# Kernel optimization log

Hardware: AMD Instinct MI355X
Metric: run time of the kernel (lower is better)

The kernel has to match this reference:

```python
import jax, jax.numpy as jnp
import numpy as np

MU = 255          # mu-law levels - 1
H = 64            # block_hidden_size
SKIP = 256        # skip_size
NL = 24           # num_layers
CYC = 6           # cycle_size -> dilation = 2**(i % CYC)
UPK = 4           # upsample conv kernel/stride
REP = 75          # upsample repeat
LF = 80           # local_features_size
B = 2
LLEN = 64                      # local (spectrogram) frames
SLEN = LLEN * UPK * REP        # 19200 signal samples


def setup_inputs() -> dict:
    key = jax.random.key(0)
    ks = jax.random.split(key, 16)
    s = 0.1
    rn = lambda k, shape: jax.random.normal(k, shape, jnp.float32) * s
    return {
        "local_features": jax.random.normal(ks[0], (B, LLEN, LF), jnp.float32),
        "gold_signal": jax.random.randint(ks[1], (B, SLEN), 0, MU + 1, jnp.int32),
        "embed_W": rn(ks[2], (H, MU + 1)),          # 1x1 conv (mu+1 -> H), as matrix
        "embed_b": rn(ks[3], (H,)),
        "up_W": rn(ks[4], (LF, LF, UPK)),           # ConvTranspose1d weight [in, out, k]
        "up_b": rn(ks[5], (LF,)),
        "cond_W": rn(ks[6], (NL * 2 * H, LF)),      # 1x1 conv LF -> NL*2H
        "cond_b": rn(ks[7], (NL * 2 * H,)),
        "dil_W": rn(ks[8], (NL, 2 * H, H, 2)),      # dilated causal conv, kernel 2
        "dil_b": rn(ks[9], (NL, 2 * H)),
        "skip_W": rn(ks[10], (NL, SKIP, H)),
        "skip_b": rn(ks[11], (NL, SKIP)),
        "res_W": rn(ks[12], (NL - 1, H, H)),        # no residual conv on last layer
        "res_b": rn(ks[13], (NL - 1, H)),
        "out_W1": rn(ks[14], (MU + 1, SKIP)),       # out conv 1 (no bias)
        "out_W2": rn(ks[15], (MU + 1, MU + 1)),     # out conv 2 (no bias)
    }


def reference(local_features, gold_signal, embed_W, embed_b, up_W, up_b,
              cond_W, cond_b, dil_W, dil_b, skip_W, skip_b, res_W, res_b,
              out_W1, out_W2):
    Bv = local_features.shape[0]
    # --- conditional features upsample ---
    x = jnp.transpose(local_features, (0, 2, 1))                     # [B, LF, Lloc]
    # ConvTranspose1d with kernel == stride == UPK: each frame emits UPK frames
    up = jnp.einsum('bct,cok->botk', x, up_W).reshape(Bv, LF, -1)    # [B, LF, Lloc*UPK]
    up = up + up_b[None, :, None]
    up = jnp.repeat(up, REP, axis=-1)                                # [B, LF, SLEN]
    cond = jnp.einsum('oc,bct->bot', cond_W, up) + cond_b[None, :, None]
    L = cond.shape[-1]
    cond = cond.reshape(Bv, NL, 2 * H, L)                            # per-layer 2H channels
    # --- embed mu-law one-hot signal (one-hot matmul == gather) ---
    sig = jnp.transpose(embed_W[:, gold_signal], (1, 0, 2)) + embed_b[None, :, None]  # [B, H, L]
    # --- residual blocks ---
    skip_sum = jnp.zeros((Bv, SKIP, L), cond.dtype)
    for i in range(NL):
        d = 2 ** (i % CYC)
        prev = jnp.pad(sig, ((0, 0), (0, 0), (d, 0)))[:, :, :L]      # causal shift by dilation
        a = (jnp.einsum('oc,bct->bot', dil_W[i, :, :, 0], prev)
             + jnp.einsum('oc,bct->bot', dil_W[i, :, :, 1], sig)
             + dil_b[i][None, :, None] + cond[:, i])
        z = jnp.tanh(a[:, :H]) * jax.nn.sigmoid(a[:, H:])            # gated activation
        skip_sum = skip_sum + jnp.einsum('oc,bct->bot', skip_W[i], z) + skip_b[i][None, :, None]
        if i < NL - 1:
            sig = sig + jnp.einsum('oc,bct->bot', res_W[i], z) + res_b[i][None, :, None]
    # --- output head: ReLU -> 1x1 -> ReLU -> 1x1 -> log_softmax over levels ---
    h = jax.nn.relu(skip_sum)
    h = jax.nn.relu(jnp.einsum('oc,bct->bot', out_W1, h))
    logits = jnp.einsum('oc,bct->bot', out_W2, h)
    return jax.nn.log_softmax(logits, axis=1)                        # [B, mu+1, SLEN]
```

## Files before the change

### kernel.cpp

```cpp
#include <hip/hip_runtime.h>
#include <math.h>

#define MU1   256
#define H     64
#define H2    128
#define SKIPC 256
#define NL    24
#define LF    80
#define UPK   4
#define REP   75
#define BB    2
#define LLEN  64
#define LL    19200

using bf16x8 = __attribute__((ext_vector_type(8))) short;
using bf16x4 = __attribute__((ext_vector_type(4))) short;
using f32x4  = __attribute__((ext_vector_type(4))) float;

__device__ __forceinline__ float b2f(short s) {
    union { unsigned u; float f; } v; v.u = ((unsigned)(unsigned short)s) << 16; return v.f;
}
__device__ __forceinline__ short f2b(float f) {
    union { float f; unsigned u; } v; v.f = f;
    unsigned r = (v.u + 0x7fff + ((v.u >> 16) & 1)) >> 16;
    return (short)r;
}

__global__ __launch_bounds__(256) void prep_kernel(
    const float* __restrict__ dil_W,  const float* __restrict__ skip_W,
    const float* __restrict__ res_W,  const float* __restrict__ embed_W,
    const float* __restrict__ embed_b,const float* __restrict__ cond_W,
    const float* __restrict__ out_W1, const float* __restrict__ out_W2,
    const float* __restrict__ skip_b,
    short* __restrict__ dil_Wb, short* __restrict__ skip_Wb,
    short* __restrict__ res_Wb, short* __restrict__ embed_allb,
    float* __restrict__ cond_Wt, short* __restrict__ W1b,
    short* __restrict__ W2b, float* __restrict__ sbsum)
{
    int idx = blockIdx.x * 256 + threadIdx.x;
    const int n1 = NL * 2 * H2 * H;
    const int n2 = NL * SKIPC * H;
    const int n3 = (NL - 1) * H * H;
    const int n4 = MU1 * H;
    const int n5 = LF * NL * H2;
    const int n6 = MU1 * SKIPC;
    const int n7 = MU1 * MU1;
    if (idx < n1) {
        int c = idx & 63; int o = (idx >> 6) & 127;
        int k = (idx >> 13) & 1; int i = idx >> 14;
        dil_Wb[idx] = f2b(dil_W[((i * H2 + o) * H + c) * 2 + k]);
        return;
    }
    idx -= n1;
    if (idx < n2) { skip_Wb[idx] = f2b(skip_W[idx]); return; }
    idx -= n2;
    if (idx < n3) { res_Wb[idx] = f2b(res_W[idx]); return; }
    idx -= n3;
    if (idx < n4) {
        int h = idx & 63; int g = idx >> 6;
        embed_allb[idx] = f2b(embed_W[h * MU1 + g] + embed_b[h]);
        return;
    }
    idx -= n4;
    if (idx < n5) {
        int o = idx % (NL * H2); int c = idx / (NL * H2);
        cond_Wt[idx] = cond_W[o * LF + c];
        return;
    }
    idx -= n5;
    if (idx < n6) { W1b[idx] = f2b(out_W1[idx]); return; }
    idx -= n6;
    if (idx < n7) { W2b[idx] = f2b(out_W2[idx]); return; }
    idx -= n7;
    if (idx < SKIPC) {
        float a = 0.f;
        for (int i = 0; i < NL; i++) a += skip_b[i * SKIPC + idx];
        sbsum[idx] = a;
        return;
    }
}

__global__ __launch_bounds__(256) void embed_kernel(
    const int* __restrict__ gold, const short* __restrict__ eW,
    short* __restrict__ sig)
{
    int idx = blockIdx.x * 256 + threadIdx.x;
    if (idx >= BB * LL * 8) return;
    int ch = idx & 7; int bt = idx >> 3;
    int g = gold[bt];
    *(bf16x8*)(sig + (size_t)bt * H + ch * 8) = *(const bf16x8*)(eW + g * H + ch * 8);
}

__global__ __launch_bounds__(256) void cond_kernel(
    const float* __restrict__ lf, const float* __restrict__ up_W,
    const float* __restrict__ up_b, const float* __restrict__ cond_Wt,
    const float* __restrict__ cond_b, const float* __restrict__ dil_b,
    float* __restrict__ condS)
{
    __shared__ float s_up[LF];
    int j = blockIdx.x;
    int ot = blockIdx.y;
    int b = blockIdx.z;
    int frame = j >> 2, k = j & 3;
    int tid = threadIdx.x;
    if (tid < LF) {
        float a = up_b[tid];
        const float* lfr = lf + (b * LLEN + frame) * LF;
        #pragma unroll 8
        for (int c = 0; c < LF; ++c) a += lfr[c] * up_W[(c * LF + tid) * UPK + k];
        s_up[tid] = a;
    }
    __syncthreads();
    int o = ot * 256 + tid;
    float a = cond_b[o] + dil_b[o];
    #pragma unroll 8
    for (int c = 0; c < LF; ++c) a += cond_Wt[c * 3072 + o] * s_up[c];
    condS[((size_t)(b * 256 + j)) * 3072 + o] = a;
}

template<bool LASTPAIR>
__global__ __launch_bounds__(256) void pair_mfma(
    const short* __restrict__ sig_in, short* __restrict__ sig_out,
    short* __restrict__ z_grp,
    const short* __restrict__ dil_Wb_all,
    const short* __restrict__ res_Wb_all,
    const float* __restrict__ res_b_all,
    const float* __restrict__ condS,
    int p, int dA, int dB)
{
    __shared__ __align__(16) short sa[144][72];
    __shared__ __align__(16) short sb[128][72];
    __shared__ __align__(16) short sz[128][72];
    __shared__ float scond[2][3][128];

    const int iA = 2 * p, iB = 2 * p + 1;
    const int b = blockIdx.y;
    const int t0 = blockIdx.x * 96;
    const int tid = threadIdx.x;
    const int w = tid >> 6;
    const int lane = tid & 63;
    const int lr = lane & 15, lg = lane >> 4;
    const int c0 = (t0 >= 32) ? (t0 - 32) / 75 : 0;

    {
        const short* basein = sig_in + (size_t)b * LL * H;
        #pragma unroll
        for (int it = 0; it < 5; ++it) {
            int task = tid + it * 256;
            if (task < 1152) {
                int r = task >> 3, ch = task & 7;
                int t = t0 - 48 + r;
                bf16x8 v = {};
                if (t >= 0) v = *(const bf16x8*)(basein + (size_t)t * H + ch * 8);
                *(bf16x8*)&sa[r][ch * 8] = v;
            }
        }
        #pragma unroll
        for (int it = 0; it < 3; ++it) {
            int task = tid + it * 256;
            int sel = task >= 384;
            int cj = (task - sel * 384) >> 7;
            int o = task & 127;
            int col = c0 + cj; col = col > 255 ? 255 : col;
            scond[sel][cj][o] = condS[((size_t)(b * 256 + col)) * 3072 + (iA + sel) * 128 + o];
        }
    }
    __syncthreads();

    {
        const short* dW = dil_Wb_all + (size_t)iA * 2 * H2 * H;
        f32x4 acc[2][8];
        #pragma unroll
        for (int m = 0; m < 2; ++m)
            #pragma unroll
            for (int n = 0; n < 8; ++n) acc[m][n] = (f32x4){0.f, 0.f, 0.f, 0.f};
        bf16x8 afA[2][4];
        #pragma unroll
        for (int m = 0; m < 2; ++m) {
            int rc = 16 + 16 * (2 * w + m) + lr;
            afA[m][0] = *(const bf16x8*)&sa[rc - dA][lg * 8];
            afA[m][1] = *(const bf16x8*)&sa[rc - dA][32 + lg * 8];
            afA[m][2] = *(const bf16x8*)&sa[rc][lg * 8];
            afA[m][3] = *(const bf16x8*)&sa[rc][32 + lg * 8];
        }
        #pragma unroll
        for (int n = 0; n < 8; ++n)
            #pragma unroll
            for (int kk = 0; kk < 4; ++kk) {
                bf16x8 bw = *(const bf16x8*)(dW + (((kk >> 1) * H2 + 16 * n + lr) * H) + (kk & 1) * 32 + lg * 8);
                acc[0][n] = __builtin_amdgcn_mfma_f32_16x16x32_bf16(afA[0][kk], bw, acc[0][n], 0, 0, 0);
                acc[1][n] = __builtin_amdgcn_mfma_f32_16x16x32_bf16(afA[1][kk], bw, acc[1][n], 0, 0, 0);
            }
        #pragma unroll
        for (int m = 0; m < 2; ++m)
            #pragma unroll
            for (int n = 0; n < 4; ++n)
                #pragma unroll
                for (int r = 0; r < 4; ++r) {
                    int relt = -32 + 16 * (2 * w + m) + 4 * lg + r;
                    int t = t0 + relt;
                    int o = 16 * n + lr;
                    short zb = 0;
                    if (t >= 0) {
                        int ci = t / 75 - c0;
                        float av = acc[m][n][r] + scond[0][ci][o];
                        float gv = acc[m][n + 4][r] + scond[0][ci][64 + o];
                        float th = 1.f - 2.f / (__expf(2.f * av) + 1.f);
                        float sg = 1.f / (1.f + __expf(-gv));
                        zb = f2b(th * sg);
                    }
                    sz[relt + 32][o] = zb;
                }
    }
    __syncthreads();

    #pragma unroll
    for (int it = 0; it < 3; ++it) {
        int task = tid + it * 256;
        int r = task >> 3, ch = task & 7;
        *(bf16x8*)(z_grp + ((size_t)(b * LL + t0 + r)) * 512 + (iA & 7) * 64 + ch * 8)
            = *(const bf16x8*)&sz[32 + r][ch * 8];
    }

    {
        const short* rW = res_Wb_all + (size_t)iA * H * H;
        const float* rb_ = res_b_all + (size_t)iA * H;
        f32x4 rac[2][4];
        #pragma unroll
        for (int m = 0; m < 2; ++m)
            #pragma unroll
            for (int n = 0; n < 4; ++n) rac[m][n] = (f32x4){0.f, 0.f, 0.f, 0.f};
        bf16x8 za[2][2];
        #pragma unroll
        for (int m = 0; m < 2; ++m) {
            int row = 16 * (2 * w + m) + lr;
            za[m][0] = *(const bf16x8*)&sz[row][lg * 8];
            za[m][1] = *(const bf16x8*)&sz[row][32 + lg * 8];
        }
        #pragma unroll
        for (int n = 0; n < 4; ++n)
            #pragma unroll
            for (int kk = 0; kk < 2; ++kk) {
                bf16x8 bw = *(const bf16x8*)(rW + (16 * n + lr) * H + kk * 32 + lg * 8);
                rac[0][n] = __builtin_amdgcn_mfma_f32_16x16x32_bf16(za[0][kk], bw, rac[0][n], 0, 0, 0);
                rac[1][n] = __builtin_amdgcn_mfma_f32_16x16x32_bf16(za[1][kk], bw, rac[1][n], 0, 0, 0);
            }
        #pragma unroll
        for (int n = 0; n < 4; ++n) {
            float rbv = rb_[16 * n + lr];
            #pragma unroll
            for (int m = 0; m < 2; ++m)
                #pragma unroll
                for (int r = 0; r < 4; ++r) {
                    int relt = -32 + 16 * (2 * w + m) + 4 * lg + r;
                    int t = t0 + relt;
                    int c = 16 * n + lr;
                    short vb = 0;
                    if (t >= 0) vb = f2b(b2f(sa[relt + 48][c]) + rac[m][n][r] + rbv);
                    sb[relt + 32][c] = vb;
                }
        }
    }
    __syncthreads();

    {
        const short* dW = dil_Wb_all + (size_t)iB * 2 * H2 * H;
        f32x4 accF[6], accG[6];
        #pragma unroll
        for (int m = 0; m < 6; ++m) { accF[m] = (f32x4){0.f,0.f,0.f,0.f}; accG[m] = (f32x4){0.f,0.f,0.f,0.f}; }
        bf16x8 bwF[4], bwG[4];
        #pragma unroll
        for (int kk = 0; kk < 4; ++kk) {
            int oF = 16 * w + lr;
            bwF[kk] = *(const bf16x8*)(dW + (((kk >> 1) * H2 + oF) * H) + (kk & 1) * 32 + lg * 8);
            bwG[kk] = *(const bf16x8*)(dW + (((kk >> 1) * H2 + 64 + oF) * H) + (kk & 1) * 32 + lg * 8);
        }
        #pragma unroll
        for (int m = 0; m < 6; ++m) {
            int rc = 32 + 16 * m + lr;
            bf16x8 af[4];
            af[0] = *(const bf16x8*)&sb[rc - dB][lg * 8];
            af[1] = *(const bf16x8*)&sb[rc - dB][32 + lg * 8];
            af[2] = *(const bf16x8*)&sb[rc][lg * 8];
            af[3] = *(const bf16x8*)&sb[rc][32 + lg * 8];
            #pragma unroll
            for (int kk = 0; kk < 4; ++kk)
                accF[m] = __builtin_amdgcn_mfma_f32_16x16x32_bf16(af[kk], bwF[kk], accF[m], 0, 0, 0);
            #pragma unroll
            for (int kk = 0; kk < 4; ++kk)
                accG[m] = __builtin_amdgcn_mfma_f32_16x16x32_bf16(af[kk], bwG[kk], accG[m], 0, 0, 0);
        }
        #pragma unroll
        for (int m = 0; m < 6; ++m)
            #pragma unroll
            for (int r = 0; r < 4; ++r) {
                int relt = 16 * m + 4 * lg + r;
                int t = t0 + relt;
                int o = 16 * w + lr;
                int ci = t / 75 - c0;
                float av = accF[m][r] + scond[1][ci][o];
                float gv = accG[m][r] + scond[1][ci][64 + o];
                float th = 1.f - 2.f / (__expf(2.f * av) + 1.f);
                float sg = 1.f / (1.f + __expf(-gv));
                sz[relt][o] = f2b(th * sg);
            }
    }
    __syncthreads();

    #pragma unroll
    for (int it = 0; it < 3; ++it) {
        int task = tid + it * 256;
        int r = task >> 3, ch = task & 7;
        *(bf16x8*)(z_grp + ((size_t)(b * LL + t0 + r)) * 512 + (iB & 7) * 64 + ch * 8)
            = *(const bf16x8*)&sz[r][ch * 8];
    }

    if (!LASTPAIR) {
        const short* rW = res_Wb_all + (size_t)iB * H * H;
        const float* rb_ = res_b_all + (size_t)iB * H;
        int c = 16 * w + lr;
        f32x4 rac[6];
        #pragma unroll
        for (int m = 0; m < 6; ++m) rac[m] = (f32x4){0.f, 0.f, 0.f, 0.f};
        bf16x8 bwR[2];
        bwR[0] = *(const bf16x8*)(rW + c * H + lg * 8);
        bwR[1] = *(const bf16x8*)(rW + c * H + 32 + lg * 8);
        #pragma unroll
        for (int m = 0; m < 6; ++m) {
            bf16x8 z0 = *(const bf16x8*)&sz[16 * m + lr][lg * 8];
            bf16x8 z1 = *(const bf16x8*)&sz[16 * m + lr][32 + lg * 8];
            rac[m] = __builtin_amdgcn_mfma_f32_16x16x32_bf16(z0, bwR[0], rac[m], 0, 0, 0);
            rac[m] = __builtin_amdgcn_mfma_f32_16x16x32_bf16(z1, bwR[1], rac[m], 0, 0, 0);
        }
        float rbv = rb_[c];
        #pragma unroll
        for (int m = 0; m < 6; ++m)
            #pragma unroll
            for (int r = 0; r < 4; ++r) {
                int relt = 16 * m + 4 * lg + r;
                sa[relt][c] = f2b(b2f(sb[relt + 32][c]) + rac[m][r] + rbv);
            }
        __syncthreads();
        #pragma unroll
        for (int it = 0; it < 3; ++it) {
            int task = tid + it * 256;
            int r = task >> 3, ch = task & 7;
            *(bf16x8*)(sig_out + ((size_t)(b * LL + t0 + r)) * H + ch * 8)
                = *(const bf16x8*)&sa[r][ch * 8];
        }
    }
}

template<bool G0>
__global__ __launch_bounds__(256) void skip_gemm(
    const short* __restrict__ z_grp, const short* __restrict__ sWb,
    float* __restrict__ skipS)
{
    __shared__ __align__(16) short s_a[64][136];
    const int b = blockIdx.y;
    const int t0 = blockIdx.x * 64;
    const int tid = threadIdx.x;
    const int w = tid >> 6;
    const int lane = tid & 63;
    const int lr = lane & 15, lg = lane >> 4;

    f32x4 acc[4][4];
    #pragma unroll
    for (int mt = 0; mt < 4; ++mt)
        #pragma unroll
        for (int nt = 0; nt < 4; ++nt) acc[mt][nt] = (f32x4){0.f, 0.f, 0.f, 0.f};

    for (int chunk = 0; chunk < 4; ++chunk) {
        __syncthreads();
        #pragma unroll
        for (int it = 0; it < 4; ++it) {
            int task = tid + it * 256;
            int r = task >> 4, ch = task & 15;
            *(bf16x8*)&s_a[r][ch * 8] =
                *(const bf16x8*)(z_grp + ((size_t)(b * LL + t0 + r)) * 512 + chunk * 128 + ch * 8);
        }
        __syncthreads();
        bf16x8 bw[4][4];
        #pragma unroll
        for (int nt = 0; nt < 4; ++nt)
            #pragma unroll
            for (int kk = 0; kk < 4; ++kk) {
                int layer = 2 * chunk + (kk >> 1);
                bw[nt][kk] = *(const bf16x8*)(sWb +
                    ((size_t)(layer * SKIPC + 64 * w + 16 * nt + lr)) * H + (kk & 1) * 32 + 8 * lg);
            }
        #pragma unroll
        for (int mt = 0; mt < 4; ++mt) {
            bf16x8 afr[4];
            #pragma unroll
            for (int kk = 0; kk < 4; ++kk)
                afr[kk] = *(const bf16x8*)&s_a[16 * mt + lr][32 * kk + 8 * lg];
            #pragma unroll
            for (int nt = 0; nt < 4; ++nt)
                #pragma unroll
                for (int kk = 0; kk < 4; ++kk)
                    acc[mt][nt] = __builtin_amdgcn_mfma_f32_16x16x32_bf16(afr[kk], bw[nt][kk], acc[mt][nt], 0, 0, 0);
        }
    }
    #pragma unroll
    for (int mt = 0; mt < 4; ++mt)
        #pragma unroll
        for (int nt = 0; nt < 4; ++nt) {
            int s = 64 * w + 16 * nt + lr;
            #pragma unroll
            for (int reg = 0; reg < 4; ++reg) {
                int t = t0 + 16 * mt + 4 * lg + reg;
                float* p = skipS + ((size_t)(b * LL + t)) * SKIPC + s;
                float v = acc[mt][nt][reg];
                if (!G0) v += *p;
                *p = v;
            }
        }
}

__global__ __launch_bounds__(256) void head_mfma(
    const float* __restrict__ skipS, const float* __restrict__ sbsum,
    const short* __restrict__ W1b, const short* __restrict__ W2b,
    float* __restrict__ out)
{
    __shared__ __align__(16) unsigned char smem[128 * 68 * 4];
    short (*s_x)[264] = (short(*)[264])smem;
    float (*s_o)[68]  = (float(*)[68])smem;
    __shared__ float s_red[4][64];
    __shared__ float s_sb[256];

    const int b = blockIdx.y;
    const int t0 = blockIdx.x * 64;
    const int tid = threadIdx.x;
    const int w = tid >> 6;
    const int lane = tid & 63;
    const int lr = lane & 15, lg = lane >> 4;

    s_sb[tid] = sbsum[tid];
    __syncthreads();

    #pragma unroll
    for (int it = 0; it < 16; ++it) {
        int task = tid + it * 256;
        int r = task >> 6, c4 = task & 63;
        f32x4 v = *(const f32x4*)(skipS + ((size_t)(b * LL + t0 + r)) * SKIPC + c4 * 4);
        bf16x4 o;
        #pragma unroll
        for (int j = 0; j < 4; ++j) o[j] = f2b(fmaxf(v[j] + s_sb[c4 * 4 + j], 0.f));
        *(bf16x4*)&s_x[r][c4 * 4] = o;
    }
    __syncthreads();

    f32x4 acc1[4][4];
    #pragma unroll
    for (int mt = 0; mt < 4; ++mt)
        #pragma unroll
        for (int nt = 0; nt < 4; ++nt) acc1[mt][nt] = (f32x4){0.f, 0.f, 0.f, 0.f};
    #pragma unroll
    for (int mt = 0; mt < 4; ++mt) {
        bf16x8 afr[8];
        #pragma unroll
        for (int kk = 0; kk < 8; ++kk)
            afr[kk] = *(const bf16x8*)&s_x[16 * mt + lr][32 * kk + 8 * lg];
        #pragma unroll
        for (int nt = 0; nt < 4; ++nt)
            #pragma unroll
            for (int kk = 0; kk < 8; ++kk) {
                bf16x8 bw = *(const bf16x8*)(W1b + ((size_t)(64 * w + 16 * nt + lr)) * MU1 + 32 * kk + 8 * lg);
                acc1[mt][nt] = __builtin_amdgcn_mfma_f32_16x16x32_bf16(afr[kk], bw, acc1[mt][nt], 0, 0, 0);
            }
    }
    __syncthreads();
    #pragma unroll
    for (int mt = 0; mt < 4; ++mt)
        #pragma unroll
        for (int nt = 0; nt < 4; ++nt)
            #pragma unroll
            for (int reg = 0; reg < 4; ++reg) {
                int tl = 16 * mt + 4 * lg + reg;
                int o = 64 * w + 16 * nt + lr;
                s_x[tl][o] = f2b(fmaxf(acc1[mt][nt][reg], 0.f));
            }
    __syncthreads();

    f32x4 acc2[4][4];
    #pragma unroll
    for (int mt = 0; mt < 4; ++mt)
        #pragma unroll
        for (int nt = 0; nt < 4; ++nt) acc2[mt][nt] = (f32x4){0.f, 0.f, 0.f, 0.f};
    #pragma unroll
    for (int mt = 0; mt < 4; ++mt) {
        bf16x8 afr[8];
        #pragma unroll
        for (int kk = 0; kk < 8; ++kk)
            afr[kk] = *(const bf16x8*)&s_x[16 * mt + lr][32 * kk + 8 * lg];
        #pragma unroll
        for (int nt = 0; nt < 4; ++nt)
            #pragma unroll
            for (int kk = 0; kk < 8; ++kk) {
                bf16x8 bw = *(const bf16x8*)(W2b + ((size_t)(64 * w + 16 * nt + lr)) * MU1 + 32 * kk + 8 * lg);
                acc2[mt][nt] = __builtin_amdgcn_mfma_f32_16x16x32_bf16(afr[kk], bw, acc2[mt][nt], 0, 0, 0);
            }
    }

    float mv[4][4];
    #pragma unroll
    for (int mt = 0; mt < 4; ++mt)
        #pragma unroll
        for (int reg = 0; reg < 4; ++reg) {
            float m = -3.4e38f;
            #pragma unroll
            for (int nt = 0; nt < 4; ++nt) m = fmaxf(m, acc2[mt][nt][reg]);
            #pragma unroll
            for (int off = 1; off <= 8; off <<= 1) m = fmaxf(m, __shfl_xor(m, off));
            int tl = 16 * mt + 4 * lg + reg;
            if (lr == 0) s_red[w][tl] = m;
        }
    __syncthreads();
    #pragma unroll
    for (int mt = 0; mt < 4; ++mt)
        #pragma unroll
        for (int reg = 0; reg < 4; ++reg) {
            int tl = 16 * mt + 4 * lg + reg;
            mv[mt][reg] = fmaxf(fmaxf(s_red[0][tl], s_red[1][tl]), fmaxf(s_red[2][tl], s_red[3][tl]));
        }
    __syncthreads();
    #pragma unroll
    for (int mt = 0; mt < 4; ++mt)
        #pragma unroll
        for (int reg = 0; reg < 4; ++reg) {
            float s = 0.f;
            #pragma unroll
            for (int nt = 0; nt < 4; ++nt) s += __expf(acc2[mt][nt][reg] - mv[mt][reg]);
            #pragma unroll
            for (int off = 1; off <= 8; off <<= 1) s += __shfl_xor(s, off);
            int tl = 16 * mt + 4 * lg + reg;
            if (lr == 0) s_red[w][tl] = s;
        }
    __syncthreads();
    #pragma unroll
    for (int mt = 0; mt < 4; ++mt)
        #pragma unroll
        for (int reg = 0; reg < 4; ++reg) {
            int tl = 16 * mt + 4 * lg + reg;
            float denom = s_red[0][tl] + s_red[1][tl] + s_red[2][tl] + s_red[3][tl];
            mv[mt][reg] = mv[mt][reg] + logf(denom);
        }
    __syncthreads();

    #pragma unroll
    for (int pass = 0; pass < 2; ++pass) {
        if ((w >> 1) == pass) {
            #pragma unroll
            for (int mt = 0; mt < 4; ++mt)
                #pragma unroll
                for (int nt = 0; nt < 4; ++nt)
                    #pragma unroll
                    for (int reg = 0; reg < 4; ++reg) {
                        int ch = 64 * (w & 1) + 16 * nt + lr;
                        int tl = 16 * mt + 4 * lg + reg;
                        s_o[ch][tl] = acc2[mt][nt][reg] - mv[mt][reg];
                    }
        }
        __syncthreads();
        {
            int row = tid >> 1, half = tid & 1;
            float* op = out + ((size_t)(b * MU1 + pass * 128 + row)) * LL + t0 + half * 32;
            #pragma unroll
            for (int k = 0; k < 8; ++k)
                *(f32x4*)(op + 4 * k) = *(const f32x4*)&s_o[row][half * 32 + 4 * k];
        }
        __syncthreads();
    }
}

extern "C" void kernel_launch(void* const* d_in, const int* in_sizes, int n_in,
                              void* d_out, int out_size, void* d_ws, size_t ws_size,
                              hipStream_t stream)
{
    const float* lf      = (const float*)d_in[0];
    const int*   gold    = (const int*)  d_in[1];
    const float* embed_W = (const float*)d_in[2];
    const float* embed_b = (const float*)d_in[3];
    const float* up_W    = (const float*)d_in[4];
    const float* up_b    = (const float*)d_in[5];
    const float* cond_W  = (const float*)d_in[6];
    const float* cond_b  = (const float*)d_in[7];
    const float* dil_W   = (const float*)d_in[8];
    const float* dil_b   = (const float*)d_in[9];
    const float* skip_W  = (const float*)d_in[10];
    const float* skip_b  = (const float*)d_in[11];
    const float* res_W   = (const float*)d_in[12];
    const float* res_b   = (const float*)d_in[13];
    const float* W1      = (const float*)d_in[14];
    const float* W2      = (const float*)d_in[15];
    float* out = (float*)d_out;

    unsigned char* p = (unsigned char*)d_ws;
    short* sigA      = (short*)p; p += (size_t)BB * LL * H * 2;
    short* sigB      = (short*)p; p += (size_t)BB * LL * H * 2;
    short* z_grp     = (short*)p; p += (size_t)BB * LL * 512 * 2;
    float* skipS     = (float*)p; p += (size_t)BB * LL * SKIPC * 4;
    float* condS     = (float*)p; p += (size_t)BB * 256 * NL * H2 * 4;
    short* dil_Wb    = (short*)p; p += (size_t)NL * 2 * H2 * H * 2;
    short* skip_Wb   = (short*)p; p += (size_t)NL * SKIPC * H * 2;
    short* res_Wb    = (short*)p; p += (size_t)(NL - 1) * H * H * 2;
    short* embed_allb= (short*)p; p += (size_t)MU1 * H * 2;
    float* cond_Wt   = (float*)p; p += (size_t)LF * NL * H2 * 4;
    short* W1b       = (short*)p; p += (size_t)MU1 * SKIPC * 2;
    short* W2b       = (short*)p; p += (size_t)MU1 * MU1 * 2;
    float* sbsum     = (float*)p; p += (size_t)SKIPC * 4;

    const int prep_n = NL*2*H2*H + NL*SKIPC*H + (NL-1)*H*H + MU1*H + LF*NL*H2 + MU1*SKIPC + MU1*MU1 + SKIPC;
    prep_kernel<<<(prep_n + 255) / 256, 256, 0, stream>>>(
        dil_W, skip_W, res_W, embed_W, embed_b, cond_W, W1, W2, skip_b,
        dil_Wb, skip_Wb, res_Wb, embed_allb, cond_Wt, W1b, W2b, sbsum);

    embed_kernel<<<(BB * LL * 8 + 255) / 256, 256, 0, stream>>>(gold, embed_allb, sigA);

    cond_kernel<<<dim3(256, 12, BB), 256, 0, stream>>>(lf, up_W, up_b, cond_Wt, cond_b, dil_b, condS);

    const int dil[6] = {1, 2, 4, 8, 16, 32};
    short* si = sigA;
    short* so = sigB;
    dim3 pgrid(LL / 96, BB);
    dim3 sgrid(LL / 64, BB);
    for (int pp = 0; pp < 12; ++pp) {
        int dA = dil[(2 * pp) % 6];
        int dB = dil[(2 * pp + 1) % 6];
        if (pp == 11)
            pair_mfma<true><<<pgrid, 256, 0, stream>>>(si, so, z_grp, dil_Wb, res_Wb, res_b, condS, pp, dA, dB);
        else
            pair_mfma<false><<<pgrid, 256, 0, stream>>>(si, so, z_grp, dil_Wb, res_Wb, res_b, condS, pp, dA, dB);
        short* tmp = si; si = so; so = tmp;

        if ((pp & 3) == 3) {
            int g = pp >> 2;
            const short* sWb = skip_Wb + (size_t)g * 8 * SKIPC * H;
            if (g == 0)
                skip_gemm<true><<<sgrid, 256, 0, stream>>>(z_grp, sWb, skipS);
            else
                skip_gemm<false><<<sgrid, 256, 0, stream>>>(z_grp, sWb, skipS);
        }
    }

    head_mfma<<<sgrid, 256, 0, stream>>>(skipS, sbsum, W1b, W2b, out);
}
```

Baseline: 577.4 us.

## Restructure skip accumulation into two 12-layer GEMMs and fuse second into head

Result: faster. 559.0 us (-3.2%).

```diff
diff --git a/kernel.cpp b/kernel.cpp
--- a/kernel.cpp
+++ b/kernel.cpp
@@ -32,14 +32,14 @@
     const float* __restrict__ embed_b,const float* __restrict__ cond_W,
     const float* __restrict__ out_W1, const float* __restrict__ out_W2,
     const float* __restrict__ skip_b,
-    short* __restrict__ dil_Wb, short* __restrict__ skip_Wb,
+    short* __restrict__ dil_Wb, short* __restrict__ sWt,
     short* __restrict__ res_Wb, short* __restrict__ embed_allb,
     float* __restrict__ cond_Wt, short* __restrict__ W1b,
     short* __restrict__ W2b, float* __restrict__ sbsum)
 {
     int idx = blockIdx.x * 256 + threadIdx.x;
     const int n1 = NL * 2 * H2 * H;
-    const int n2 = NL * SKIPC * H;
+    const int n2 = 12 * 256 * 128;
     const int n3 = (NL - 1) * H * H;
     const int n4 = MU1 * H;
     const int n5 = LF * NL * H2;
@@ -52,7 +52,11 @@
         return;
     }
     idx -= n1;
-    if (idx < n2) { skip_Wb[idx] = f2b(skip_W[idx]); return; }
+    if (idx < n2) {
+        int kc = idx & 127; int s = (idx >> 7) & 255; int ck = idx >> 15;
+        sWt[idx] = f2b(skip_W[((2 * ck + (kc >> 6)) * SKIPC + s) * H + (kc & 63)]);
+        return;
+    }
     idx -= n2;
     if (idx < n3) { res_Wb[idx] = f2b(res_W[idx]); return; }
     idx -= n3;
@@ -118,15 +122,15 @@
     condS[((size_t)(b * 256 + j)) * 3072 + o] = a;
 }
 
-template<bool LASTPAIR>
+template<int DA, int DB, bool LASTPAIR>
 __global__ __launch_bounds__(256) void pair_mfma(
     const short* __restrict__ sig_in, short* __restrict__ sig_out,
-    short* __restrict__ z_grp,
+    short* __restrict__ z12,
     const short* __restrict__ dil_Wb_all,
     const short* __restrict__ res_Wb_all,
     const float* __restrict__ res_b_all,
     const float* __restrict__ condS,
-    int p, int dA, int dB)
+    int p, int slot)
 {
     __shared__ __align__(16) short sa[144][72];
     __shared__ __align__(16) short sb[128][72];
@@ -178,8 +182,8 @@
         #pragma unroll
         for (int m = 0; m < 2; ++m) {
             int rc = 16 + 16 * (2 * w + m) + lr;
-            afA[m][0] = *(const bf16x8*)&sa[rc - dA][lg * 8];
-            afA[m][1] = *(const bf16x8*)&sa[rc - dA][32 + lg * 8];
+            afA[m][0] = *(const bf16x8*)&sa[rc - DA][lg * 8];
+            afA[m][1] = *(const bf16x8*)&sa[rc - DA][32 + lg * 8];
             afA[m][2] = *(const bf16x8*)&sa[rc][lg * 8];
             afA[m][3] = *(const bf16x8*)&sa[rc][32 + lg * 8];
         }
@@ -218,7 +222,7 @@
     for (int it = 0; it < 3; ++it) {
         int task = tid + it * 256;
         int r = task >> 3, ch = task & 7;
-        *(bf16x8*)(z_grp + ((size_t)(b * LL + t0 + r)) * 512 + (iA & 7) * 64 + ch * 8)
+        *(bf16x8*)(z12 + ((size_t)((slot * BB + b) * LL) + t0 + r) * 128 + ch * 8)
             = *(const bf16x8*)&sz[32 + r][ch * 8];
     }
 
@@ -279,8 +283,8 @@
         for (int m = 0; m < 6; ++m) {
             int rc = 32 + 16 * m + lr;
             bf16x8 af[4];
-            af[0] = *(const bf16x8*)&sb[rc - dB][lg * 8];
-            af[1] = *(const bf16x8*)&sb[rc - dB][32 + lg * 8];
+            af[0] = *(const bf16x8*)&sb[rc - DB][lg * 8];
+            af[1] = *(const bf16x8*)&sb[rc - DB][32 + lg * 8];
             af[2] = *(const bf16x8*)&sb[rc][lg * 8];
             af[3] = *(const bf16x8*)&sb[rc][32 + lg * 8];
             #pragma unroll
@@ -311,7 +315,7 @@
     for (int it = 0; it < 3; ++it) {
         int task = tid + it * 256;
         int r = task >> 3, ch = task & 7;
-        *(bf16x8*)(z_grp + ((size_t)(b * LL + t0 + r)) * 512 + (iB & 7) * 64 + ch * 8)
+        *(bf16x8*)(z12 + ((size_t)((slot * BB + b) * LL) + t0 + r) * 128 + 64 + ch * 8)
             = *(const bf16x8*)&sz[r][ch * 8];
     }
 
@@ -351,12 +355,11 @@
     }
 }
 
-template<bool G0>
-__global__ __launch_bounds__(256) void skip_gemm(
-    const short* __restrict__ z_grp, const short* __restrict__ sWb,
-    float* __restrict__ skipS)
+__global__ __launch_bounds__(256) void skip12_kernel(
+    const short* __restrict__ z12, const short* __restrict__ sWt,
+    short* __restrict__ skipP)
 {
-    __shared__ __align__(16) short s_a[64][136];
+    __shared__ __align__(16) short s_a[2][64][136];
     const int b = blockIdx.y;
     const int t0 = blockIdx.x * 64;
     const int tid = threadIdx.x;
@@ -370,38 +373,44 @@
         #pragma unroll
         for (int nt = 0; nt < 4; ++nt) acc[mt][nt] = (f32x4){0.f, 0.f, 0.f, 0.f};
 
-    for (int chunk = 0; chunk < 4; ++chunk) {
+    #pragma unroll
+    for (int it = 0; it < 4; ++it) {
+        int task = tid + it * 256;
+        int r = task >> 4, ch = task & 15;
+        *(bf16x8*)&s_a[0][r][ch * 8] =
+            *(const bf16x8*)(z12 + ((size_t)(b * LL) + t0 + r) * 128 + ch * 8);
+    }
+    __syncthreads();
+
+    for (int ck = 0; ck < 6; ++ck) {
+        if (ck < 5) {
+            #pragma unroll
+            for (int it = 0; it < 4; ++it) {
+                int task = tid + it * 256;
+                int r = task >> 4, ch = task & 15;
+                *(bf16x8*)&s_a[(ck + 1) & 1][r][ch * 8] =
+                    *(const bf16x8*)(z12 + ((size_t)(((ck + 1) * BB + b) * LL) + t0 + r) * 128 + ch * 8);
+            }
+        }
+        const short* wbase = sWt + ((size_t)ck << 15);
+        const short (*buf)[136] = s_a[ck & 1];
+        #pragma unroll
+        for (int kk = 0; kk < 4; ++kk) {
+            bf16x8 afr[4];
+            #pragma unroll
+            for (int mt = 0; mt < 4; ++mt)
+                afr[mt] = *(const bf16x8*)&buf[16 * mt + lr][32 * kk + 8 * lg];
+            #pragma unroll
+            for (int nt = 0; nt < 4; ++nt) {
+                bf16x8 bw = *(const bf16x8*)(wbase + ((64 * w + 16 * nt + lr) << 7) + 32 * kk + 8 * lg);
+                #pragma unroll
+                for (int mt = 0; mt < 4; ++mt)
+                    acc[mt][nt] = __builtin_amdgcn_mfma_f32_16x16x32_bf16(afr[mt], bw, acc[mt][nt], 0, 0, 0);
+            }
+        }
         __syncthreads();
-        #pragma unroll
-        for (int it = 0; it < 4; ++it) {
-            int task = tid + it * 256;
-            int r = task >> 4, ch = task & 15;
-            *(bf16x8*)&s_a[r][ch * 8] =
-                *(const bf16x8*)(z_grp + ((size_t)(b * LL + t0 + r)) * 512 + chunk * 128 + ch * 8);
-        }
-        __syncthreads();
-        bf16x8 bw[4][4];
-        #pragma unroll
-        for (int nt = 0; nt < 4; ++nt)
-            #pragma unroll
-            for (int kk = 0; kk < 4; ++kk) {
-                int layer = 2 * chunk + (kk >> 1);
-                bw[nt][kk] = *(const bf16x8*)(sWb +
-                    ((size_t)(layer * SKIPC + 64 * w + 16 * nt + lr)) * H + (kk & 1) * 32 + 8 * lg);
-            }
-        #pragma unroll
-        for (int mt = 0; mt < 4; ++mt) {
-            bf16x8 afr[4];
-            #pragma unroll
-            for (int kk = 0; kk < 4; ++kk)
-                afr[kk] = *(const bf16x8*)&s_a[16 * mt + lr][32 * kk + 8 * lg];
-            #pragma unroll
-            for (int nt = 0; nt < 4; ++nt)
-                #pragma unroll
-                for (int kk = 0; kk < 4; ++kk)
-                    acc[mt][nt] = __builtin_amdgcn_mfma_f32_16x16x32_bf16(afr[kk], bw[nt][kk], acc[mt][nt], 0, 0, 0);
-        }
-    }
+    }
+
     #pragma unroll
     for (int mt = 0; mt < 4; ++mt)
         #pragma unroll
@@ -410,20 +419,19 @@
             #pragma unroll
             for (int reg = 0; reg < 4; ++reg) {
                 int t = t0 + 16 * mt + 4 * lg + reg;
-                float* p = skipS + ((size_t)(b * LL + t)) * SKIPC + s;
-                float v = acc[mt][nt][reg];
-                if (!G0) v += *p;
-                *p = v;
-            }
-        }
-}
-
-__global__ __launch_bounds__(256) void head_mfma(
-    const float* __restrict__ skipS, const float* __restrict__ sbsum,
+                skipP[((size_t)(b * LL) + t) * 256 + s] = f2b(acc[mt][nt][reg]);
+            }
+        }
+}
+
+__global__ __launch_bounds__(256) void skiphead_kernel(
+    const short* __restrict__ z12, const short* __restrict__ sWt,
+    const short* __restrict__ skipP, const float* __restrict__ sbsum,
     const short* __restrict__ W1b, const short* __restrict__ W2b,
     float* __restrict__ out)
 {
-    __shared__ __align__(16) unsigned char smem[128 * 68 * 4];
+    __shared__ __align__(16) unsigned char smem[36864];
+    short (*s_ab)[64][136] = (short(*)[64][136])smem;
     short (*s_x)[264] = (short(*)[264])smem;
     float (*s_o)[68]  = (float(*)[68])smem;
     __shared__ float s_red[4][64];
@@ -437,18 +445,70 @@
     const int lr = lane & 15, lg = lane >> 4;
 
     s_sb[tid] = sbsum[tid];
-    __syncthreads();
-
-    #pragma unroll
-    for (int it = 0; it < 16; ++it) {
+
+    f32x4 acc[4][4];
+    #pragma unroll
+    for (int mt = 0; mt < 4; ++mt)
+        #pragma unroll
+        for (int nt = 0; nt < 4; ++nt) acc[mt][nt] = (f32x4){0.f, 0.f, 0.f, 0.f};
+
+    #pragma unroll
+    for (int it = 0; it < 4; ++it) {
         int task = tid + it * 256;
-        int r = task >> 6, c4 = task & 63;
-        f32x4 v = *(const f32x4*)(skipS + ((size_t)(b * LL + t0 + r)) * SKIPC + c4 * 4);
-        bf16x4 o;
-        #pragma unroll
-        for (int j = 0; j < 4; ++j) o[j] = f2b(fmaxf(v[j] + s_sb[c4 * 4 + j], 0.f));
-        *(bf16x4*)&s_x[r][c4 * 4] = o;
-    }
+        int r = task >> 4, ch = task & 15;
+        *(bf16x8*)&s_ab[0][r][ch * 8] =
+            *(const bf16x8*)(z12 + ((size_t)(b * LL) + t0 + r) * 128 + ch * 8);
+    }
+    __syncthreads();
+    for (int ck = 0; ck < 6; ++ck) {
+        if (ck < 5) {
+            #pragma unroll
+            for (int it = 0; it < 4; ++it) {
+                int task = tid + it * 256;
+                int r = task >> 4, ch = task & 15;
+                *(bf16x8*)&s_ab[(ck + 1) & 1][r][ch * 8] =
+                    *(const bf16x8*)(z12 + ((size_t)(((ck + 1) * BB + b) * LL) + t0 + r) * 128 + ch * 8);
+            }
+        }
+        const short* wbase = sWt + ((size_t)(6 + ck) << 15);
+        const short (*buf)[136] = s_ab[ck & 1];
+        #pragma unroll
+        for (int kk = 0; kk < 4; ++kk) {
+            bf16x8 afr[4];
+            #pragma unroll
+            for (int mt = 0; mt < 4; ++mt)
+                afr[mt] = *(const bf16x8*)&buf[16 * mt + lr][32 * kk + 8 * lg];
+            #pragma unroll
+            for (int nt = 0; nt < 4; ++nt) {
+                bf16x8 bw = *(const bf16x8*)(wbase + ((64 * w + 16 * nt + lr) << 7) + 32 * kk + 8 * lg);
+                #pragma unroll
+                for (int mt = 0; mt < 4; ++mt)
+                    acc[mt][nt] = __builtin_amdgcn_mfma_f32_16x16x32_bf16(afr[mt], bw, acc[mt][nt], 0, 0, 0);
+            }
+        }
+        __syncthreads();
+    }
+
+    #pragma unroll
+    for (int it = 0; it < 8; ++it) {
+        int task = tid + it * 256;
+        int r = task >> 5, ch = task & 31;
+        *(bf16x8*)&s_x[r][ch * 8] =
+            *(const bf16x8*)(skipP + ((size_t)(b * LL) + t0 + r) * 256 + ch * 8);
+    }
+    __syncthreads();
+    #pragma unroll
+    for (int mt = 0; mt < 4; ++mt)
+        #pragma unroll
+        for (int nt = 0; nt < 4; ++nt) {
+            int s = 64 * w + 16 * nt + lr;
+            #pragma unroll
+            for (int reg = 0; reg < 4; ++reg) {
+                int tl = 16 * mt + 4 * lg + reg;
+                float v = acc[mt][nt][reg] + b2f(s_x[tl][s]) + s_sb[s];
+                s_x[tl][s] = f2b(fmaxf(v, 0.f));
+            }
+        }
     __syncthreads();
 
     f32x4 acc1[4][4];
@@ -457,18 +517,18 @@
         #pragma unroll
         for (int nt = 0; nt < 4; ++nt) acc1[mt][nt] = (f32x4){0.f, 0.f, 0.f, 0.f};
     #pragma unroll
-    for (int mt = 0; mt < 4; ++mt) {
-        bf16x8 afr[8];
-        #pragma unroll
-        for (int kk = 0; kk < 8; ++kk)
-            afr[kk] = *(const bf16x8*)&s_x[16 * mt + lr][32 * kk + 8 * lg];
-        #pragma unroll
-        for (int nt = 0; nt < 4; ++nt)
-            #pragma unroll
-            for (int kk = 0; kk < 8; ++kk) {
-                bf16x8 bw = *(const bf16x8*)(W1b + ((size_t)(64 * w + 16 * nt + lr)) * MU1 + 32 * kk + 8 * lg);
-                acc1[mt][nt] = __builtin_amdgcn_mfma_f32_16x16x32_bf16(afr[kk], bw, acc1[mt][nt], 0, 0, 0);
-            }
+    for (int kk = 0; kk < 8; ++kk) {
+        bf16x8 afr[4];
+        #pragma unroll
+        for (int mt = 0; mt < 4; ++mt)
+            afr[mt] = *(const bf16x8*)&s_x[16 * mt + lr][32 * kk + 8 * lg];
+        #pragma unroll
+        for (int nt = 0; nt < 4; ++nt) {
+            bf16x8 bw = *(const bf16x8*)(W1b + ((size_t)(64 * w + 16 * nt + lr)) * MU1 + 32 * kk + 8 * lg);
+            #pragma unroll
+            for (int mt = 0; mt < 4; ++mt)
+                acc1[mt][nt] = __builtin_amdgcn_mfma_f32_16x16x32_bf16(afr[mt], bw, acc1[mt][nt], 0, 0, 0);
+        }
     }
     __syncthreads();
     #pragma unroll
@@ -489,18 +549,18 @@
         #pragma unroll
         for (int nt = 0; nt < 4; ++nt) acc2[mt][nt] = (f32x4){0.f, 0.f, 0.f, 0.f};
     #pragma unroll
-    for (int mt = 0; mt < 4; ++mt) {
-        bf16x8 afr[8];
-        #pragma unroll
-        for (int kk = 0; kk < 8; ++kk)
-            afr[kk] = *(const bf16x8*)&s_x[16 * mt + lr][32 * kk + 8 * lg];
-        #pragma unroll
-        for (int nt = 0; nt < 4; ++nt)
-            #pragma unroll
-            for (int kk = 0; kk < 8; ++kk) {
-                bf16x8 bw = *(const bf16x8*)(W2b + ((size_t)(64 * w + 16 * nt + lr)) * MU1 + 32 * kk + 8 * lg);
-                acc2[mt][nt] = __builtin_amdgcn_mfma_f32_16x16x32_bf16(afr[kk], bw, acc2[mt][nt], 0, 0, 0);
-            }
+    for (int kk = 0; kk < 8; ++kk) {
+        bf16x8 afr[4];
+        #pragma unroll
+        for (int mt = 0; mt < 4; ++mt)
+            afr[mt] = *(const bf16x8*)&s_x[16 * mt + lr][32 * kk + 8 * lg];
+        #pragma unroll
+        for (int nt = 0; nt < 4; ++nt) {
+            bf16x8 bw = *(const bf16x8*)(W2b + ((size_t)(64 * w + 16 * nt + lr)) * MU1 + 32 * kk + 8 * lg);
+            #pragma unroll
+            for (int mt = 0; mt < 4; ++mt)
+                acc2[mt][nt] = __builtin_amdgcn_mfma_f32_16x16x32_bf16(afr[mt], bw, acc2[mt][nt], 0, 0, 0);
+        }
     }
 
     float mv[4][4];
@@ -544,7 +604,7 @@
         for (int reg = 0; reg < 4; ++reg) {
             int tl = 16 * mt + 4 * lg + reg;
             float denom = s_red[0][tl] + s_red[1][tl] + s_red[2][tl] + s_red[3][tl];
-            mv[mt][reg] = mv[mt][reg] + logf(denom);
+            mv[mt][reg] = mv[mt][reg] + __logf(denom);
         }
     __syncthreads();
 
@@ -599,11 +659,11 @@
     unsigned char* p = (unsigned char*)d_ws;
     short* sigA      = (short*)p; p += (size_t)BB * LL * H * 2;
     short* sigB      = (short*)p; p += (size_t)BB * LL * H * 2;
-    short* z_grp     = (short*)p; p += (size_t)BB * LL * 512 * 2;
-    float* skipS     = (float*)p; p += (size_t)BB * LL * SKIPC * 4;
+    short* z12       = (short*)p; p += (size_t)6 * BB * LL * 128 * 2;
+    short* skipP     = (short*)p; p += (size_t)BB * LL * SKIPC * 2;
     float* condS     = (float*)p; p += (size_t)BB * 256 * NL * H2 * 4;
     short* dil_Wb    = (short*)p; p += (size_t)NL * 2 * H2 * H * 2;
-    short* skip_Wb   = (short*)p; p += (size_t)NL * SKIPC * H * 2;
+    short* sWt       = (short*)p; p += (size_t)12 * 256 * 128 * 2;
     short* res_Wb    = (short*)p; p += (size_t)(NL - 1) * H * H * 2;
     short* embed_allb= (short*)p; p += (size_t)MU1 * H * 2;
     float* cond_Wt   = (float*)p; p += (size_t)LF * NL * H2 * 4;
@@ -611,38 +671,35 @@
     short* W2b       = (short*)p; p += (size_t)MU1 * MU1 * 2;
     float* sbsum     = (float*)p; p += (size_t)SKIPC * 4;
 
-    const int prep_n = NL*2*H2*H + NL*SKIPC*H + (NL-1)*H*H + MU1*H + LF*NL*H2 + MU1*SKIPC + MU1*MU1 + SKIPC;
+    const int prep_n = NL*2*H2*H + 12*256*128 + (NL-1)*H*H + MU1*H + LF*NL*H2 + MU1*SKIPC + MU1*MU1 + SKIPC;
     prep_kernel<<<(prep_n + 255) / 256, 256, 0, stream>>>(
         dil_W, skip_W, res_W, embed_W, embed_b, cond_W, W1, W2, skip_b,
-        dil_Wb, skip_Wb, res_Wb, embed_allb, cond_Wt, W1b, W2b, sbsum);
+        dil_Wb, sWt, res_Wb, embed_allb, cond_Wt, W1b, W2b, sbsum);
 
     embed_kernel<<<(BB * LL * 8 + 255) / 256, 256, 0, stream>>>(gold, embed_allb, sigA);
 
     cond_kernel<<<dim3(256, 12, BB), 256, 0, stream>>>(lf, up_W, up_b, cond_Wt, cond_b, dil_b, condS);
 
-    const int dil[6] = {1, 2, 4, 8, 16, 32};
     short* si = sigA;
     short* so = sigB;
     dim3 pgrid(LL / 96, BB);
     dim3 sgrid(LL / 64, BB);
     for (int pp = 0; pp < 12; ++pp) {
-        int dA = dil[(2 * pp) % 6];
-        int dB = dil[(2 * pp + 1) % 6];
-        if (pp == 11)
-            pair_mfma<true><<<pgrid, 256, 0, stream>>>(si, so, z_grp, dil_Wb, res_Wb, res_b, condS, pp, dA, dB);
+        int slot = pp % 6;
+        int r3 = pp % 3;
+        if (r3 == 0)
+            pair_mfma<1, 2, false><<<pgrid, 256, 0, stream>>>(si, so, z12, dil_Wb, res_Wb, res_b, condS, pp, slot);
+        else if (r3 == 1)
+            pair_mfma<4, 8, false><<<pgrid, 256, 0, stream>>>(si, so, z12, dil_Wb, res_Wb, res_b, condS, pp, slot);
+        else if (pp == 11)
+            pair_mfma<16, 32, true><<<pgrid, 256, 0, stream>>>(si, so, z12, dil_Wb, res_Wb, res_b, condS, pp, slot);
         else
-            pair_mfma<false><<<pgrid, 256, 0, stream>>>(si, so, z_grp, dil_Wb, res_Wb, res_b, condS, pp, dA, dB);
+            pair_mfma<16, 32, false><<<pgrid, 256, 0, stream>>>(si, so, z12, dil_Wb, res_Wb, res_b, condS, pp, slot);
         short* tmp = si; si = so; so = tmp;
 
-        if ((pp & 3) == 3) {
-            int g = pp >> 2;
-            const short* sWb = skip_Wb + (size_t)g * 8 * SKIPC * H;
-            if (g == 0)
-                skip_gemm<true><<<sgrid, 256, 0, stream>>>(z_grp, sWb, skipS);
-            else
-                skip_gemm<false><<<sgrid, 256, 0, stream>>>(z_grp, sWb, skipS);
-        }
-    }
-
-    head_mfma<<<sgrid, 256, 0, stream>>>(skipS, sbsum, W1b, W2b, out);
-}
+        if (pp == 5)
+            skip12_kernel<<<sgrid, 256, 0, stream>>>(z12, sWt, skipP);
+    }
+
+    skiphead_kernel<<<sgrid, 256, 0, stream>>>(z12, sWt, skipP, sbsum, W1b, W2b, out);
+}
```
